# Performance work log

Hardware: AMD Instinct MI355X
Metric: run time of the kernel (lower is better)

## Reference

```python
import jax, jax.numpy as jnp
import numpy as np

KERNEL_MUL = [2.0, 2.0]
KERNEL_NUM = [5, 1]
FIX_SIGMA = [None, 1.68]


def setup_inputs() -> dict:
    key = jax.random.key(0)
    k0, k1, k2, k3 = jax.random.split(key, 4)
    B, D0, D1 = 4096, 2048, 128
    return {
        "src_f0": jax.random.normal(k0, (B, D0), dtype=jnp.float32),
        "src_f1": jax.random.normal(k1, (B, D1), dtype=jnp.float32),
        "tar_f0": jax.random.normal(k2, (B, D0), dtype=jnp.float32),
        "tar_f1": jax.random.normal(k3, (B, D1), dtype=jnp.float32),
    }


def _gaussian_kernel(src, tar, kernel_mul, kernel_num, fix_sigma):
    n_samples = src.shape[0] + tar.shape[0]
    total = jnp.concatenate([src, tar], axis=0)  # [2B, D]
    # pairwise squared L2 distance without the O(N^2*D) expanded intermediate
    sq = jnp.sum(total * total, axis=1)
    l2 = sq[:, None] + sq[None, :] - 2.0 * (total @ total.T)  # [2B, 2B]
    if fix_sigma:
        bandwidth = jnp.asarray(fix_sigma, dtype=l2.dtype)
    else:
        # original uses L2_distance.data (detached) for the bandwidth estimate
        bandwidth = jax.lax.stop_gradient(jnp.sum(l2)) / (n_samples ** 2 - n_samples)
    bandwidth = bandwidth / (kernel_mul ** (kernel_num // 2))
    kernel = jnp.zeros_like(l2)
    for i in range(kernel_num):
        kernel = kernel + jnp.exp(-l2 / (bandwidth * kernel_mul ** i))
    return kernel


def reference(src_f0, src_f1, tar_f0, tar_f1):
    src_list = [src_f0, src_f1]
    tar_list = [tar_f0, tar_f1]
    joint = None
    for i in range(len(src_list)):
        k = _gaussian_kernel(src_list[i], tar_list[i], KERNEL_MUL[i], KERNEL_NUM[i], FIX_SIGMA[i])
        joint = k if joint is None else joint * k
    B = src_f0.shape[0]
    XX = joint[:B, :B]
    YY = joint[B:, B:]
    XY = joint[:B, B:]
    YX = joint[B:, :B]
    return jnp.mean(XX + YY - XY - YX)
```

## Files before the change

### kernel.cpp

```cpp
#include <hip/hip_runtime.h>
#include <stdint.h>

#define B_ROWS 4096
#define NTOT   8192
#define D0     2048
#define D1     128
#define TAU    112.0f

#define OFF_ACC   0
#define OFF_S0    8
#define OFF_BW    16
#define OFF_CNT   20
#define OFF_DONE  24
#define OFF_M0    32
#define OFF_SQ1   8320
#define OFF_T1    41216
#define OFF_CAND  2138368
#define ZERO_WORDS 2056

typedef _Float16 half8 __attribute__((ext_vector_type(8)));
typedef _Float16 half2v __attribute__((ext_vector_type(2)));
typedef float f32x4 __attribute__((ext_vector_type(4)));

__global__ void p0a(const float* __restrict__ src1, const float* __restrict__ tar1, char* __restrict__ ws) {
    if (blockIdx.x == 0) {
        unsigned* w = (unsigned*)ws;
        for (int i = threadIdx.x; i < ZERO_WORDS; i += 256) w[i] = 0;
    }
    int wave = threadIdx.x >> 6, lane = threadIdx.x & 63;
    int row = blockIdx.x * 4 + wave;
    const float2* rp = (const float2*)(row < B_ROWS ? src1 + (size_t)row * D1
                                                    : tar1 + (size_t)(row - B_ROWS) * D1);
    float2 v = rp[lane];
    float sq = v.x * v.x + v.y * v.y;
    #pragma unroll
    for (int off = 32; off; off >>= 1) sq += __shfl_down(sq, off);
    if (lane == 0) ((float*)(ws + OFF_SQ1))[row] = sq;
    half2v h; h[0] = (_Float16)v.x; h[1] = (_Float16)v.y;
    ((half2v*)(ws + OFF_T1))[(size_t)row * 64 + lane] = h;
}

__global__ __launch_bounds__(256, 4) void phaseA(char* __restrict__ ws, unsigned cap) {
    int tid = blockIdx.x;
    int bi = (int)((129.0 - sqrt(129.0 * 129.0 - 8.0 * (double)tid)) * 0.5);
    while (((bi + 1) * (129 - (bi + 1))) / 2 <= tid) bi++;
    while ((bi * (129 - bi)) / 2 > tid) bi--;
    int bj = bi + (tid - (bi * (129 - bi)) / 2);

    const char* t1 = (const char*)(ws + OFF_T1);
    int t = threadIdx.x;
    int lane = t & 63, wave = t >> 6;
    int wm = wave & 1, wn = wave >> 1;
    int quad = lane >> 4;
    int Abase = bi * 128, Bbase = bj * 128;

    const char* aptr = t1 + (((size_t)(Abase + wm * 64 + (lane & 15))) << 8) + quad * 16;
    const char* bptr = t1 + (((size_t)(Bbase + wn * 64 + (lane & 15))) << 8) + quad * 16;

    f32x4 acc[4][4];
    #pragma unroll
    for (int i = 0; i < 4; i++)
        #pragma unroll
        for (int j = 0; j < 4; j++) acc[i][j] = (f32x4){0.f, 0.f, 0.f, 0.f};

    #pragma unroll
    for (int ks = 0; ks < 4; ks++) {
        half8 af[4], bf[4];
        #pragma unroll
        for (int mi = 0; mi < 4; mi++)
            af[mi] = *(const half8*)(aptr + mi * 4096 + ks * 64);
        #pragma unroll
        for (int nj = 0; nj < 4; nj++)
            bf[nj] = *(const half8*)(bptr + nj * 4096 + ks * 64);
        #pragma unroll
        for (int mi = 0; mi < 4; mi++)
            #pragma unroll
            for (int nj = 0; nj < 4; nj++)
                acc[mi][nj] = __builtin_amdgcn_mfma_f32_16x16x32_f16(
                    af[mi], bf[nj], acc[mi][nj], 0, 0, 0);
    }

    const float* sq1 = (const float*)(ws + OFF_SQ1);
    unsigned* cnt = (unsigned*)(ws + OFF_CNT);
    uint2* cand = (uint2*)(ws + OFF_CAND);
    f32x4 sqa[4];
    #pragma unroll
    for (int mi = 0; mi < 4; mi++)
        sqa[mi] = *(const f32x4*)&sq1[Abase + wm * 64 + mi * 16 + quad * 4];
    #pragma unroll
    for (int nj = 0; nj < 4; nj++) {
        int b = Bbase + wn * 64 + nj * 16 + (lane & 15);
        float sqb = sq1[b];
        #pragma unroll
        for (int mi = 0; mi < 4; mi++) {
            int abase = Abase + wm * 64 + mi * 16 + quad * 4;
            #pragma unroll
            for (int r = 0; r < 4; r++) {
                int a = abase + r;
                float l2 = sqa[mi][r] + sqb - 2.0f * acc[mi][nj][r];
                if (l2 < TAU && a < b) {
                    unsigned idx = atomicAdd(cnt, 1u);
                    if (idx < cap) cand[idx] = make_uint2((unsigned)a, (unsigned)b);
                }
            }
        }
    }
}

__global__ void bwk1(const float* __restrict__ src0, const float* __restrict__ tar0, char* __restrict__ ws) {
    if (*(volatile unsigned*)(ws + OFF_CNT) == 0) return;
    int d4 = blockIdx.x * 256 + threadIdx.x;
    int rbase = blockIdx.y * 64;
    const float4* base = (const float4*)(rbase < B_ROWS ? src0 + (size_t)rbase * D0
                                                        : tar0 + (size_t)(rbase - B_ROWS) * D0);
    float4 cs = {0.f, 0.f, 0.f, 0.f};
    float sq = 0.f;
    for (int r = 0; r < 64; r++) {
        float4 v = base[(size_t)r * 512 + d4];
        cs.x += v.x; cs.y += v.y; cs.z += v.z; cs.w += v.w;
        sq += v.x * v.x + v.y * v.y + v.z * v.z + v.w * v.w;
    }
    float* m0 = (float*)(ws + OFF_M0);
    atomicAdd(&m0[d4 * 4 + 0], cs.x);
    atomicAdd(&m0[d4 * 4 + 1], cs.y);
    atomicAdd(&m0[d4 * 4 + 2], cs.z);
    atomicAdd(&m0[d4 * 4 + 3], cs.w);
    #pragma unroll
    for (int off = 32; off; off >>= 1) sq += __shfl_down(sq, off);
    __shared__ float red[4];
    int lane = threadIdx.x & 63, wave = threadIdx.x >> 6;
    if (lane == 0) red[wave] = sq;
    __syncthreads();
    if (threadIdx.x == 0)
        atomicAdd((double*)(ws + OFF_S0), (double)(red[0] + red[1] + red[2] + red[3]));
}

__global__ void phaseB(const float* __restrict__ src0, const float* __restrict__ src1,
                       const float* __restrict__ tar0, const float* __restrict__ tar1,
                       char* __restrict__ ws, unsigned cap, float* __restrict__ out) {
    __shared__ double red[4];
    __shared__ float fred[4];
    __shared__ float bws;
    unsigned cnt = *(const unsigned*)(ws + OFF_CNT);
    if (cnt > cap) cnt = cap;
    int lane = threadIdx.x & 63, wave = threadIdx.x >> 6;
    if (cnt > 0) {
        const float* m0 = (const float*)(ws + OFF_M0);
        float s = 0.f;
        for (int j = threadIdx.x; j < 2048; j += 256) { float v = m0[j]; s += v * v; }
        #pragma unroll
        for (int off = 32; off; off >>= 1) s += __shfl_down(s, off);
        if (lane == 0) fred[wave] = s;
        __syncthreads();
        if (threadIdx.x == 0) {
            double m2 = (double)fred[0] + fred[1] + fred[2] + fred[3];
            double S0 = *(double*)(ws + OFF_S0);
            double lsum2 = 2.0 * (double)NTOT * S0 - 2.0 * m2;
            bws = (float)(lsum2 / ((double)NTOT * NTOT - NTOT) / 4.0);
        }
        __syncthreads();
        float bw = bws;
        const uint2* cand = (const uint2*)(ws + OFF_CAND);
        unsigned gw = blockIdx.x * 4 + wave;
        unsigned nw = gridDim.x * 4;
        double lsum = 0.0;
        for (unsigned i = gw; i < cnt; i += nw) {
            uint2 p = cand[i];
            unsigned a = p.x, b = p.y;
            const float* ra0 = a < B_ROWS ? src0 + (size_t)a * D0 : tar0 + (size_t)(a - B_ROWS) * D0;
            const float* rb0 = b < B_ROWS ? src0 + (size_t)b * D0 : tar0 + (size_t)(b - B_ROWS) * D0;
            const float* ra1 = a < B_ROWS ? src1 + (size_t)a * D1 : tar1 + (size_t)(a - B_ROWS) * D1;
            const float* rb1 = b < B_ROWS ? src1 + (size_t)b * D1 : tar1 + (size_t)(b - B_ROWS) * D1;
            float d1;
            {
                float2 x = ((const float2*)ra1)[lane];
                float2 y = ((const float2*)rb1)[lane];
                float dx = x.x - y.x, dy = x.y - y.y;
                d1 = dx * dx + dy * dy;
            }
            float d0 = 0.f;
            #pragma unroll
            for (int j = 0; j < 8; j++) {
                float4 x = ((const float4*)ra0)[lane + 64 * j];
                float4 y = ((const float4*)rb0)[lane + 64 * j];
                float dx = x.x - y.x, dy = x.y - y.y, dz = x.z - y.z, dw = x.w - y.w;
                d0 += dx * dx + dy * dy + dz * dz + dw * dw;
            }
            #pragma unroll
            for (int off = 32; off; off >>= 1) {
                d0 += __shfl_down(d0, off);
                d1 += __shfl_down(d1, off);
            }
            if (lane == 0) {
                float k1 = expf(-d1 / 1.68f);
                float k0 = 0.f, bwj = bw;
                #pragma unroll
                for (int j = 0; j < 5; j++) { k0 += expf(-d0 / bwj); bwj *= 2.0f; }
                float sgn = ((a < B_ROWS) == (b < B_ROWS)) ? 1.0f : -1.0f;
                lsum += (double)(2.0f * sgn * k0 * k1);
            }
        }
        if (lane == 0) red[wave] = lsum;
        __syncthreads();
        if (threadIdx.x == 0)
            atomicAdd((double*)(ws + OFF_ACC), red[0] + red[1] + red[2] + red[3]);
    }
    __threadfence();
    if (threadIdx.x == 0) {
        unsigned d = atomicAdd((unsigned*)(ws + OFF_DONE), 1u);
        if (d == gridDim.x - 1) {
            double acc = atomicAdd((double*)(ws + OFF_ACC), 0.0);
            out[0] = (float)((acc + (double)NTOT * 5.0) / ((double)B_ROWS * (double)B_ROWS));
        }
    }
}

extern "C" void kernel_launch(void* const* d_in, const int* in_sizes, int n_in,
                              void* d_out, int out_size, void* d_ws, size_t ws_size,
                              hipStream_t stream) {
    const float* src0 = (const float*)d_in[0];
    const float* src1 = (const float*)d_in[1];
    const float* tar0 = (const float*)d_in[2];
    const float* tar1 = (const float*)d_in[3];
    char* ws = (char*)d_ws;
    unsigned cap = 0;
    if (ws_size > (size_t)OFF_CAND + 8) {
        size_t c = (ws_size - OFF_CAND) / 8;
        if (c > (size_t)4 * 1024 * 1024) c = (size_t)4 * 1024 * 1024;
        cap = (unsigned)c;
    }
    p0a<<<2048, 256, 0, stream>>>(src1, tar1, ws);
    phaseA<<<2080, 256, 0, stream>>>(ws, cap);
    bwk1<<<dim3(2, 128), 256, 0, stream>>>(src0, tar0, ws);
    phaseB<<<64, 256, 0, stream>>>(src0, src1, tar0, tar1, ws, cap, (float*)d_out);
}
```

Before: 139.7 us.

## Fuse fp16 conversion and row norms into phaseA via shared-memory tiles

```diff
diff --git a/kernel.cpp b/kernel.cpp
--- a/kernel.cpp
+++ b/kernel.cpp
@@ -13,49 +13,86 @@
 #define OFF_CNT   20
 #define OFF_DONE  24
 #define OFF_M0    32
-#define OFF_SQ1   8320
-#define OFF_T1    41216
 #define OFF_CAND  2138368
 #define ZERO_WORDS 2056
 
 typedef _Float16 half8 __attribute__((ext_vector_type(8)));
-typedef _Float16 half2v __attribute__((ext_vector_type(2)));
 typedef float f32x4 __attribute__((ext_vector_type(4)));
 
-__global__ void p0a(const float* __restrict__ src1, const float* __restrict__ tar1, char* __restrict__ ws) {
-    if (blockIdx.x == 0) {
-        unsigned* w = (unsigned*)ws;
-        for (int i = threadIdx.x; i < ZERO_WORDS; i += 256) w[i] = 0;
-    }
-    int wave = threadIdx.x >> 6, lane = threadIdx.x & 63;
-    int row = blockIdx.x * 4 + wave;
-    const float2* rp = (const float2*)(row < B_ROWS ? src1 + (size_t)row * D1
-                                                    : tar1 + (size_t)(row - B_ROWS) * D1);
-    float2 v = rp[lane];
-    float sq = v.x * v.x + v.y * v.y;
-    #pragma unroll
-    for (int off = 32; off; off >>= 1) sq += __shfl_down(sq, off);
-    if (lane == 0) ((float*)(ws + OFF_SQ1))[row] = sq;
-    half2v h; h[0] = (_Float16)v.x; h[1] = (_Float16)v.y;
-    ((half2v*)(ws + OFF_T1))[(size_t)row * 64 + lane] = h;
-}
-
-__global__ __launch_bounds__(256, 4) void phaseA(char* __restrict__ ws, unsigned cap) {
+#define LDST 136
+
+__global__ void zerok(char* __restrict__ ws) {
+    unsigned* w = (unsigned*)ws;
+    for (int i = threadIdx.x; i < ZERO_WORDS; i += 256) w[i] = 0;
+}
+
+__global__ __launch_bounds__(256) void phaseA(const float* __restrict__ src1,
+                                              const float* __restrict__ tar1,
+                                              char* __restrict__ ws, unsigned cap) {
     int tid = blockIdx.x;
     int bi = (int)((129.0 - sqrt(129.0 * 129.0 - 8.0 * (double)tid)) * 0.5);
     while (((bi + 1) * (129 - (bi + 1))) / 2 <= tid) bi++;
     while ((bi * (129 - bi)) / 2 > tid) bi--;
     int bj = bi + (tid - (bi * (129 - bi)) / 2);
 
-    const char* t1 = (const char*)(ws + OFF_T1);
+    __shared__ __align__(16) _Float16 At[128 * LDST];
+    __shared__ __align__(16) _Float16 Bt[128 * LDST];
+    __shared__ float sqA[128], sqB[128];
+
     int t = threadIdx.x;
     int lane = t & 63, wave = t >> 6;
     int wm = wave & 1, wn = wave >> 1;
     int quad = lane >> 4;
     int Abase = bi * 128, Bbase = bj * 128;
 
-    const char* aptr = t1 + (((size_t)(Abase + wm * 64 + (lane & 15))) << 8) + quad * 16;
-    const char* bptr = t1 + (((size_t)(Bbase + wn * 64 + (lane & 15))) << 8) + quad * 16;
+    int r = t >> 1, h = t & 1;
+    {
+        int row = Abase + r;
+        const float4* rp = (const float4*)((row < B_ROWS ? src1 + (size_t)row * D1
+                                                         : tar1 + (size_t)(row - B_ROWS) * D1) + h * 64);
+        float4 v[16];
+        #pragma unroll
+        for (int j = 0; j < 16; j++) v[j] = rp[j];
+        float sq = 0.f;
+        #pragma unroll
+        for (int j = 0; j < 16; j++)
+            sq += v[j].x * v[j].x + v[j].y * v[j].y + v[j].z * v[j].z + v[j].w * v[j].w;
+        sq += __shfl_xor(sq, 1);
+        if (h == 0) sqA[r] = sq;
+        #pragma unroll
+        for (int j = 0; j < 8; j++) {
+            half8 o;
+            o[0] = (_Float16)v[2 * j].x;     o[1] = (_Float16)v[2 * j].y;
+            o[2] = (_Float16)v[2 * j].z;     o[3] = (_Float16)v[2 * j].w;
+            o[4] = (_Float16)v[2 * j + 1].x; o[5] = (_Float16)v[2 * j + 1].y;
+            o[6] = (_Float16)v[2 * j + 1].z; o[7] = (_Float16)v[2 * j + 1].w;
+            *(half8*)((char*)At + r * (LDST * 2) + h * 128 + j * 16) = o;
+        }
+    }
+    {
+        int row = Bbase + r;
+        const float4* rp = (const float4*)((row < B_ROWS ? src1 + (size_t)row * D1
+                                                         : tar1 + (size_t)(row - B_ROWS) * D1) + h * 64);
+        float4 v[16];
+        #pragma unroll
+        for (int j = 0; j < 16; j++) v[j] = rp[j];
+        float sq = 0.f;
+        #pragma unroll
+        for (int j = 0; j < 16; j++)
+            sq += v[j].x * v[j].x + v[j].y * v[j].y + v[j].z * v[j].z + v[j].w * v[j].w;
+        sq += __shfl_xor(sq, 1);
+        if (h == 0) sqB[r] = sq;
+        #pragma unroll
+        for (int j = 0; j < 8; j++) {
+            half8 o;
+            o[0] = (_Float16)v[2 * j].x;     o[1] = (_Float16)v[2 * j].y;
+            o[2] = (_Float16)v[2 * j].z;     o[3] = (_Float16)v[2 * j].w;
+            o[4] = (_Float16)v[2 * j + 1].x; o[5] = (_Float16)v[2 * j + 1].y;
+            o[6] = (_Float16)v[2 * j + 1].z; o[7] = (_Float16)v[2 * j + 1].w;
+            *(half8*)((char*)Bt + r * (LDST * 2) + h * 128 + j * 16) = o;
+        }
+    }
+    __syncthreads();
 
     f32x4 acc[4][4];
     #pragma unroll
@@ -65,13 +102,18 @@
 
     #pragma unroll
     for (int ks = 0; ks < 4; ks++) {
+        int koffB = ks * 64 + quad * 16;
         half8 af[4], bf[4];
         #pragma unroll
-        for (int mi = 0; mi < 4; mi++)
-            af[mi] = *(const half8*)(aptr + mi * 4096 + ks * 64);
-        #pragma unroll
-        for (int nj = 0; nj < 4; nj++)
-            bf[nj] = *(const half8*)(bptr + nj * 4096 + ks * 64);
+        for (int mi = 0; mi < 4; mi++) {
+            int row = wm * 64 + mi * 16 + (lane & 15);
+            af[mi] = *(const half8*)((const char*)At + row * (LDST * 2) + koffB);
+        }
+        #pragma unroll
+        for (int nj = 0; nj < 4; nj++) {
+            int row = wn * 64 + nj * 16 + (lane & 15);
+            bf[nj] = *(const half8*)((const char*)Bt + row * (LDST * 2) + koffB);
+        }
         #pragma unroll
         for (int mi = 0; mi < 4; mi++)
             #pragma unroll
@@ -80,24 +122,24 @@
                     af[mi], bf[nj], acc[mi][nj], 0, 0, 0);
     }
 
-    const float* sq1 = (const float*)(ws + OFF_SQ1);
     unsigned* cnt = (unsigned*)(ws + OFF_CNT);
     uint2* cand = (uint2*)(ws + OFF_CAND);
     f32x4 sqa[4];
     #pragma unroll
     for (int mi = 0; mi < 4; mi++)
-        sqa[mi] = *(const f32x4*)&sq1[Abase + wm * 64 + mi * 16 + quad * 4];
+        sqa[mi] = *(const f32x4*)&sqA[wm * 64 + mi * 16 + quad * 4];
     #pragma unroll
     for (int nj = 0; nj < 4; nj++) {
-        int b = Bbase + wn * 64 + nj * 16 + (lane & 15);
-        float sqb = sq1[b];
+        int bl = wn * 64 + nj * 16 + (lane & 15);
+        int b = Bbase + bl;
+        float sqb = sqB[bl];
         #pragma unroll
         for (int mi = 0; mi < 4; mi++) {
             int abase = Abase + wm * 64 + mi * 16 + quad * 4;
             #pragma unroll
-            for (int r = 0; r < 4; r++) {
-                int a = abase + r;
-                float l2 = sqa[mi][r] + sqb - 2.0f * acc[mi][nj][r];
+            for (int rr = 0; rr < 4; rr++) {
+                int a = abase + rr;
+                float l2 = sqa[mi][rr] + sqb - 2.0f * acc[mi][nj][rr];
                 if (l2 < TAU && a < b) {
                     unsigned idx = atomicAdd(cnt, 1u);
                     if (idx < cap) cand[idx] = make_uint2((unsigned)a, (unsigned)b);
@@ -229,8 +271,8 @@
         if (c > (size_t)4 * 1024 * 1024) c = (size_t)4 * 1024 * 1024;
         cap = (unsigned)c;
     }
-    p0a<<<2048, 256, 0, stream>>>(src1, tar1, ws);
-    phaseA<<<2080, 256, 0, stream>>>(ws, cap);
+    zerok<<<1, 256, 0, stream>>>(ws);
+    phaseA<<<2080, 256, 0, stream>>>(src1, tar1, ws, cap);
     bwk1<<<dim3(2, 128), 256, 0, stream>>>(src0, tar0, ws);
     phaseB<<<64, 256, 0, stream>>>(src0, src1, tar0, tar1, ws, cap, (float*)d_out);
 }
```

Result: no change. 142.4 us (+1.9%).
